# Kernel optimization log

Measured on AMD Instinct MI355X. Metric: run time of the kernel, lower is better.

## Reference

```python
import jax, jax.numpy as jnp
import numpy as np

D_MODEL = 1024
N_HEADS = 16
D_K = D_MODEL // N_HEADS


def setup_inputs() -> dict:
    key = jax.random.key(0)
    ks = jax.random.split(key, 9)
    B, S = 4, 2048
    scale = 0.02
    x = jax.random.normal(ks[0], (B, S, D_MODEL), dtype=jnp.float32)
    mask = jnp.ones((1, 1, S, S), dtype=jnp.int32)
    wq = jax.random.normal(ks[1], (D_MODEL, D_MODEL), dtype=jnp.float32) * scale
    bq = jnp.zeros((D_MODEL,), dtype=jnp.float32)
    wk = jax.random.normal(ks[2], (D_MODEL, D_MODEL), dtype=jnp.float32) * scale
    bk = jnp.zeros((D_MODEL,), dtype=jnp.float32)
    wv = jax.random.normal(ks[3], (D_MODEL, D_MODEL), dtype=jnp.float32) * scale
    bv = jnp.zeros((D_MODEL,), dtype=jnp.float32)
    wo = jax.random.normal(ks[4], (D_MODEL, D_MODEL), dtype=jnp.float32) * scale
    bo = jnp.zeros((D_MODEL,), dtype=jnp.float32)
    return {"x": x, "mask": mask, "wq": wq, "bq": bq, "wk": wk, "bk": bk,
            "wv": wv, "bv": bv, "wo": wo, "bo": bo}


def reference(x, mask, wq, bq, wk, bk, wv, bv, wo, bo):
    B, S, _ = x.shape
    # torch Linear: y = x @ W.T + b
    def proj(w, b):
        return (jnp.einsum('bsd,ed->bse', x, w) + b).reshape(B, S, N_HEADS, D_K).transpose(0, 2, 1, 3)
    q = proj(wq, bq)  # [B,H,S,Dk]
    k = proj(wk, bk)
    v = proj(wv, bv)
    scores = jnp.einsum('bhqd,bhkd->bhqk', q, k) / jnp.sqrt(jnp.float32(D_K))
    scores = jnp.where(mask == 0, jnp.float32(-jnp.inf), scores)
    attn = jax.nn.softmax(scores, axis=-1)
    out = jnp.einsum('bhqk,bhkd->bhqd', attn, v)  # [B,H,S,Dk]
    out = out.transpose(0, 2, 1, 3).reshape(B, S, D_MODEL)
    return jnp.einsum('bsd,ed->bse', out, wo) + bo
```

## Files before the change

kernel.cpp:

```cpp
#include <hip/hip_runtime.h>
#include <hip/hip_bf16.h>
#include <math.h>
#include <stdint.h>

typedef unsigned short u16;
typedef unsigned int u32;
typedef __bf16 bf16x2 __attribute__((ext_vector_type(2)));
typedef __bf16 bf16x8 __attribute__((ext_vector_type(8)));
typedef float f32x4 __attribute__((ext_vector_type(4)));

#define AS1 __attribute__((address_space(1)))
#define AS3 __attribute__((address_space(3)))

#define QSCALE 0.18033688011112042f

__device__ __forceinline__ u16 f2bf(float f) {
  union { float f; u32 i; } c; c.f = f;
  const u32 x = c.i;
  return (u16)((x + 0x7fffu + ((x >> 16) & 1u)) >> 16);
}
#if __has_builtin(__builtin_amdgcn_cvt_pk_bf16_f32)
__device__ __forceinline__ u32 pkbf(float a, float b) {
  const bf16x2 v = __builtin_amdgcn_cvt_pk_bf16_f32(a, b);
  union { bf16x2 v; u32 i; } c; c.v = v; return c.i;
}
#else
__device__ __forceinline__ u32 pkbf(float a, float b) {
  return (u32)f2bf(a) | ((u32)f2bf(b) << 16);
}
#endif
#if __has_builtin(__builtin_amdgcn_exp2f)
#define EXP2(x) __builtin_amdgcn_exp2f(x)
#else
#define EXP2(x) __expf((x) * 0.6931471805599453f)
#endif
__device__ __forceinline__ void gload_lds16(const void* g, void* lds) {
  __builtin_amdgcn_global_load_lds((const AS1 void*)g, (AS3 void*)lds, 16, 0, 0);
}

__global__ void cast_all_kernel(const float* __restrict__ x, const float* __restrict__ wq,
                                const float* __restrict__ wk, const float* __restrict__ wv,
                                const float* __restrict__ wo, u16* __restrict__ xh,
                                u16* __restrict__ wh) {
  const int i = blockIdx.x * 256 + threadIdx.x;
  const float* src; u16* dst; int off;
  if (i < 2097152) {
    src = x; dst = xh; off = i;
  } else {
    const int j = i - 2097152;
    const int w = j >> 18;
    off = j & 262143;
    src = (w == 0) ? wq : (w == 1) ? wk : (w == 2) ? wv : wo;
    dst = wh + (size_t)w * 1048576;
  }
  const float4 v = ((const float4*)src)[off];
  ushort4 o;
  o.x = f2bf(v.x); o.y = f2bf(v.y); o.z = f2bf(v.z); o.w = f2bf(v.w);
  ((ushort4*)dst)[off] = o;
}

template <int MODE, bool SCALE>
__device__ __forceinline__ void gemm_body(const u16* __restrict__ A,
                                          const u16* __restrict__ W,
                                          const float* __restrict__ bias,
                                          void* __restrict__ out) {
  __shared__ alignas(16) u16 As[128 * 32];
  __shared__ alignas(16) u16 Bs[128 * 32];
  const int tid = threadIdx.x;
  const int wave = tid >> 6, lane = tid & 63;
  const int quad = lane >> 4, l16 = lane & 15;
  const int lid = blockIdx.y * 8 + blockIdx.x;
  const int flat = ((lid & 7) << 6) | (lid >> 3);
  const int m0 = (flat >> 3) * 128, n0 = (flat & 7) * 128;
  const int wm = (wave >> 1) * 64, wn = (wave & 1) * 64;

  f32x4 vzero = {0.f, 0.f, 0.f, 0.f};
  f32x4 acc[4][4];
#pragma unroll
  for (int i = 0; i < 4; i++)
#pragma unroll
    for (int j = 0; j < 4; j++) acc[i][j] = vzero;

  for (int k0 = 0; k0 < 1024; k0 += 32) {
#pragma unroll
    for (int p = 0; p < 2; ++p) {
      const int cbase = p * 256 + wave * 64;
      const int c = cbase + lane;
      const int row = c >> 2, kc4 = c & 3;
      gload_lds16(A + (size_t)(m0 + row) * 1024 + k0 + kc4 * 8, (char*)As + cbase * 16);
      gload_lds16(W + (size_t)(n0 + row) * 1024 + k0 + kc4 * 8, (char*)Bs + cbase * 16);
    }
    __syncthreads();
    bf16x8 af[4], bw[4];
#pragma unroll
    for (int im = 0; im < 4; im++)
      af[im] = *(const bf16x8*)&As[(wm + im * 16 + l16) * 32 + quad * 8];
#pragma unroll
    for (int in_ = 0; in_ < 4; in_++)
      bw[in_] = *(const bf16x8*)&Bs[(wn + in_ * 16 + l16) * 32 + quad * 8];
#pragma unroll
    for (int im = 0; im < 4; im++)
#pragma unroll
      for (int in_ = 0; in_ < 4; in_++)
        acc[im][in_] = __builtin_amdgcn_mfma_f32_16x16x32_bf16(af[im], bw[in_], acc[im][in_], 0, 0, 0);
    __syncthreads();
  }

#pragma unroll
  for (int in_ = 0; in_ < 4; in_++) {
    const int col = n0 + wn + in_ * 16 + l16;
    const float bvf = bias[col];
    if (MODE == 2) {
      const int h = col >> 6, dk = col & 63;
#pragma unroll
      for (int im = 0; im < 4; im++) {
        const int row0 = m0 + wm + im * 16 + quad * 4;
        const int b = row0 >> 11, s = row0 & 2047;
        const u32 lo = pkbf(acc[im][in_][0] + bvf, acc[im][in_][1] + bvf);
        const u32 hi = pkbf(acc[im][in_][2] + bvf, acc[im][in_][3] + bvf);
        u16* base = (u16*)out + ((size_t)(b * 16 + h) * 64 + dk) * 2048 + s;
        uint2 pkd; pkd.x = lo; pkd.y = hi;
        *(uint2*)base = pkd;
      }
    } else {
#pragma unroll
      for (int im = 0; im < 4; im++) {
#pragma unroll
        for (int r = 0; r < 4; r++) {
          const int row = m0 + wm + im * 16 + quad * 4 + r;
          float v = acc[im][in_][r] + bvf;
          if (SCALE) v *= QSCALE;
          if (MODE == 0) {
            ((float*)out)[(size_t)row * 1024 + col] = v;
          } else {
            const int b = row >> 11, s = row & 2047;
            const int h = col >> 6, dk = col & 63;
            ((u16*)out)[((((size_t)b * 16 + h) * 2048) + s) * 64 + dk] = f2bf(v);
          }
        }
      }
    }
  }
}

__global__ __launch_bounds__(256) void gemm_qkv_kernel(
    const u16* __restrict__ x, const u16* __restrict__ wq, const u16* __restrict__ wk,
    const u16* __restrict__ wv, const float* __restrict__ bq, const float* __restrict__ bk,
    const float* __restrict__ bv, u16* __restrict__ Q, u16* __restrict__ K,
    u16* __restrict__ VT) {
  if (blockIdx.z == 0)      gemm_body<1, true >(x, wq, bq, Q);
  else if (blockIdx.z == 1) gemm_body<1, false>(x, wk, bk, K);
  else                      gemm_body<2, false>(x, wv, bv, VT);
}

__global__ __launch_bounds__(256) void gemm_o_kernel(const u16* __restrict__ A,
                                                     const u16* __restrict__ wo,
                                                     const float* __restrict__ bo,
                                                     float* __restrict__ out) {
  gemm_body<0, false>(A, wo, bo, out);
}

__global__ void mask_check_kernel(const int* __restrict__ mask, int* __restrict__ flag) {
  const int i = blockIdx.x * 256 + threadIdx.x;
  const int4 v = ((const int4*)mask)[i];
  if (v.x == 0 || v.y == 0 || v.z == 0 || v.w == 0) atomicOr(flag, 1);
}

__global__ __launch_bounds__(256) void attn_kernel(const u16* __restrict__ Q,
                                                   const u16* __restrict__ K,
                                                   const u16* __restrict__ VT,
                                                   const int* __restrict__ mask,
                                                   const int* __restrict__ flag,
                                                   u16* __restrict__ O) {
  __shared__ alignas(16) u16 Ks[64 * 64];
  __shared__ alignas(16) u16 Vt[64 * 64];
  __shared__ alignas(16) u16 Ps[4 * 2048];

  const int tid = threadIdx.x;
  const int wave = tid >> 6, lane = tid & 63;
  const int quad = lane >> 4, l16 = lane & 15;
  const int lid = blockIdx.y * 16 + blockIdx.x;
  const int flat = ((lid & 7) << 7) | (lid >> 3);
  const int qt_ = flat & 15, bh = flat >> 4;
  const int b = bh >> 4, h = bh & 15;
  const int q0 = qt_ * 128;
  const u16* Qh = Q + (size_t)bh * 2048 * 64;
  const u16* Kh = K + (size_t)bh * 2048 * 64;
  const u16* Vth = VT + (size_t)bh * 64 * 2048;
  u16* Pw = Ps + wave * 2048;
  const bool masked = (*flag != 0);

  bf16x8 aq[2][2];
#pragma unroll
  for (int qt = 0; qt < 2; qt++) {
    const u16* qrow = Qh + (size_t)(q0 + qt * 64 + wave * 16 + l16) * 64 + quad * 8;
    aq[qt][0] = *(const bf16x8*)qrow;
    aq[qt][1] = *(const bf16x8*)(qrow + 32);
  }

  f32x4 vzero = {0.f, 0.f, 0.f, 0.f};
  f32x4 acc[2][4];
#pragma unroll
  for (int qt = 0; qt < 2; qt++)
#pragma unroll
    for (int jd = 0; jd < 4; jd++) acc[qt][jd] = vzero;
  float lp[2][4] = {{0.f, 0.f, 0.f, 0.f}, {0.f, 0.f, 0.f, 0.f}};

  for (int kb = 0; kb < 32; ++kb) {
    const int key0 = kb * 64;
#pragma unroll
    for (int p = 0; p < 2; ++p) {
      const int cbase = p * 256 + wave * 64;
      const int c = cbase + lane;
      const int row = c >> 3, cc = c & 7;
      gload_lds16(Kh + (size_t)(key0 + row) * 64 + ((cc ^ (row & 7)) << 3),
                  (char*)Ks + cbase * 16);
      gload_lds16(Vth + (size_t)row * 2048 + key0 + ((cc ^ (row & 7)) << 3),
                  (char*)Vt + cbase * 16);
    }
    __syncthreads();

#pragma unroll
    for (int jn = 0; jn < 4; jn++) {
      f32x4 sc0 = vzero, sc1 = vzero;
      __builtin_amdgcn_s_setprio(1);
#pragma unroll
      for (int kc = 0; kc < 2; kc++) {
        const int r_ = jn * 16 + l16;
        const bf16x8 bk_ = *(const bf16x8*)
            &Ks[r_ * 64 + (((kc * 4 + quad) ^ (l16 & 7)) << 3)];
        sc0 = __builtin_amdgcn_mfma_f32_16x16x32_bf16(aq[0][kc], bk_, sc0, 0, 0, 0);
        sc1 = __builtin_amdgcn_mfma_f32_16x16x32_bf16(aq[1][kc], bk_, sc1, 0, 0, 0);
      }
      __builtin_amdgcn_s_setprio(0);
      if (masked) {
#pragma unroll
        for (int r = 0; r < 4; r++) {
          const int kg = key0 + jn * 16 + l16;
          const int qa = q0 + wave * 16 + quad * 4 + r;
          if (mask[(size_t)qa * 2048 + kg] == 0) sc0[r] = -INFINITY;
          if (mask[(size_t)(qa + 64) * 2048 + kg] == 0) sc1[r] = -INFINITY;
        }
      }
      float pe0[4], pe1[4];
#pragma unroll
      for (int r = 0; r < 4; r++) {
        pe0[r] = EXP2(sc0[r]); lp[0][r] += pe0[r];
        pe1[r] = EXP2(sc1[r]); lp[1][r] += pe1[r];
      }
#pragma unroll
      for (int r = 0; r < 4; r += 2) {
        const u32 pk0 = pkbf(pe0[r], pe0[r + 1]);
        const u32 pk1 = pkbf(pe1[r], pe1[r + 1]);
        const int qa = quad * 4 + r, qb = qa + 1;
        const int sw = jn * 2 + (l16 >> 3), lo3 = l16 & 7;
        Pw[qa * 64 + (((sw ^ (qa & 7)) << 3)) + lo3] = (u16)pk0;
        Pw[qb * 64 + (((sw ^ (qb & 7)) << 3)) + lo3] = (u16)(pk0 >> 16);
        Pw[(16 + qa) * 64 + (((sw ^ (qa & 7)) << 3)) + lo3] = (u16)pk1;
        Pw[(16 + qb) * 64 + (((sw ^ (qb & 7)) << 3)) + lo3] = (u16)(pk1 >> 16);
      }
    }

    bf16x8 ap0[2], ap1[2];
#pragma unroll
    for (int kc = 0; kc < 2; kc++) {
      ap0[kc] = *(const bf16x8*)&Pw[l16 * 64 + (((kc * 4 + quad) ^ (l16 & 7)) << 3)];
      ap1[kc] = *(const bf16x8*)&Pw[(16 + l16) * 64 + (((kc * 4 + quad) ^ (l16 & 7)) << 3)];
    }
    __builtin_amdgcn_s_setprio(1);
#pragma unroll
    for (int jd = 0; jd < 4; jd++) {
#pragma unroll
      for (int kc = 0; kc < 2; kc++) {
        const int dk_ = jd * 16 + l16;
        const bf16x8 bv_ = *(const bf16x8*)
            &Vt[dk_ * 64 + (((kc * 4 + quad) ^ (l16 & 7)) << 3)];
        acc[0][jd] = __builtin_amdgcn_mfma_f32_16x16x32_bf16(ap0[kc], bv_, acc[0][jd], 0, 0, 0);
        acc[1][jd] = __builtin_amdgcn_mfma_f32_16x16x32_bf16(ap1[kc], bv_, acc[1][jd], 0, 0, 0);
      }
    }
    __builtin_amdgcn_s_setprio(0);
    __syncthreads();
  }

#pragma unroll
  for (int qt = 0; qt < 2; qt++) {
#pragma unroll
    for (int r = 0; r < 4; r++) {
      float ls = lp[qt][r];
#pragma unroll
      for (int off = 1; off < 16; off <<= 1) ls += __shfl_xor(ls, off, 16);
      const float linv = 1.0f / ls;
      const int qg = q0 + qt * 64 + wave * 16 + quad * 4 + r;
      const size_t token = (size_t)b * 2048 + qg;
#pragma unroll
      for (int jd = 0; jd < 4; jd++) {
        const int col = h * 64 + jd * 16 + l16;
        O[token * 1024 + col] = f2bf(acc[qt][jd][r] * linv);
      }
    }
  }
}

extern "C" void kernel_launch(void* const* d_in, const int* in_sizes, int n_in,
                              void* d_out, int out_size, void* d_ws, size_t ws_size,
                              hipStream_t stream) {
  const float* x  = (const float*)d_in[0];
  const int* mask = (const int*)d_in[1];
  const float* wq = (const float*)d_in[2];
  const float* bq = (const float*)d_in[3];
  const float* wk = (const float*)d_in[4];
  const float* bk = (const float*)d_in[5];
  const float* wv = (const float*)d_in[6];
  const float* bv = (const float*)d_in[7];
  const float* wo = (const float*)d_in[8];
  const float* bo = (const float*)d_in[9];
  float* out = (float*)d_out;

  u16* xh = (u16*)d_ws;
  u16* wh = xh + 8388608;
  u16* Qw = wh + 4194304;
  u16* Kw = Qw + 8388608;
  u16* Vw = Kw + 8388608;
  int* mflag = (int*)(Vw + 8388608);
  u16* Ow = xh;

  hipMemsetAsync(mflag, 0, sizeof(int), stream);
  mask_check_kernel<<<4096, 256, 0, stream>>>(mask, mflag);
  cast_all_kernel<<<12288, 256, 0, stream>>>(x, wq, wk, wv, wo, xh, wh);

  gemm_qkv_kernel<<<dim3(8, 64, 3), 256, 0, stream>>>(
      xh, wh + 0 * 1048576, wh + 1 * 1048576, wh + 2 * 1048576,
      bq, bk, bv, Qw, Kw, Vw);
  attn_kernel<<<dim3(16, 64), 256, 0, stream>>>(Qw, Kw, Vw, mask, mflag, Ow);
  gemm_o_kernel<<<dim3(8, 64, 1), 256, 0, stream>>>(Ow, wh + 3 * 1048576, bo, out);
}
```

Measured before the change: 325.9 us.

## Deepen GEMM K-tile to 64 with XOR-swizzled LDS and fuse mask check into cast

The GEMM k-step grows from 32 to 64, which halves the number of barrier pairs per K loop. LDS rows are now XOR-swizzled in 16-byte chunks to avoid bank conflicts on the wider rows. The separate mask-check kernel is folded into the cast kernel as extra blocks, removing one launch. In exchange LDS use doubles per GEMM block, which may reduce occupancy.

```diff
diff --git a/kernel.cpp b/kernel.cpp
--- a/kernel.cpp
+++ b/kernel.cpp
@@ -40,9 +40,15 @@
 
 __global__ void cast_all_kernel(const float* __restrict__ x, const float* __restrict__ wq,
                                 const float* __restrict__ wk, const float* __restrict__ wv,
-                                const float* __restrict__ wo, u16* __restrict__ xh,
-                                u16* __restrict__ wh) {
+                                const float* __restrict__ wo, const int* __restrict__ mask,
+                                u16* __restrict__ xh, u16* __restrict__ wh,
+                                int* __restrict__ flag) {
   const int i = blockIdx.x * 256 + threadIdx.x;
+  if (i >= 3145728) {
+    const int4 v = ((const int4*)mask)[i - 3145728];
+    if (v.x == 0 || v.y == 0 || v.z == 0 || v.w == 0) atomicOr(flag, 1);
+    return;
+  }
   const float* src; u16* dst; int off;
   if (i < 2097152) {
     src = x; dst = xh; off = i;
@@ -64,8 +70,8 @@
                                           const u16* __restrict__ W,
                                           const float* __restrict__ bias,
                                           void* __restrict__ out) {
-  __shared__ alignas(16) u16 As[128 * 32];
-  __shared__ alignas(16) u16 Bs[128 * 32];
+  __shared__ alignas(16) u16 As[128 * 64];
+  __shared__ alignas(16) u16 Bs[128 * 64];
   const int tid = threadIdx.x;
   const int wave = tid >> 6, lane = tid & 63;
   const int quad = lane >> 4, l16 = lane & 15;
@@ -81,28 +87,36 @@
 #pragma unroll
     for (int j = 0; j < 4; j++) acc[i][j] = vzero;
 
-  for (int k0 = 0; k0 < 1024; k0 += 32) {
-#pragma unroll
-    for (int p = 0; p < 2; ++p) {
+  for (int k0 = 0; k0 < 1024; k0 += 64) {
+#pragma unroll
+    for (int p = 0; p < 4; ++p) {
       const int cbase = p * 256 + wave * 64;
       const int c = cbase + lane;
-      const int row = c >> 2, kc4 = c & 3;
-      gload_lds16(A + (size_t)(m0 + row) * 1024 + k0 + kc4 * 8, (char*)As + cbase * 16);
-      gload_lds16(W + (size_t)(n0 + row) * 1024 + k0 + kc4 * 8, (char*)Bs + cbase * 16);
+      const int row = c >> 3, cc = c & 7;
+      const int gcol = k0 + ((cc ^ (row & 7)) << 3);
+      gload_lds16(A + (size_t)(m0 + row) * 1024 + gcol, (char*)As + cbase * 16);
+      gload_lds16(W + (size_t)(n0 + row) * 1024 + gcol, (char*)Bs + cbase * 16);
     }
     __syncthreads();
-    bf16x8 af[4], bw[4];
-#pragma unroll
-    for (int im = 0; im < 4; im++)
-      af[im] = *(const bf16x8*)&As[(wm + im * 16 + l16) * 32 + quad * 8];
-#pragma unroll
-    for (int in_ = 0; in_ < 4; in_++)
-      bw[in_] = *(const bf16x8*)&Bs[(wn + in_ * 16 + l16) * 32 + quad * 8];
-#pragma unroll
-    for (int im = 0; im < 4; im++)
-#pragma unroll
-      for (int in_ = 0; in_ < 4; in_++)
-        acc[im][in_] = __builtin_amdgcn_mfma_f32_16x16x32_bf16(af[im], bw[in_], acc[im][in_], 0, 0, 0);
+#pragma unroll
+    for (int kk = 0; kk < 2; kk++) {
+      bf16x8 af[4], bw[4];
+#pragma unroll
+      for (int im = 0; im < 4; im++) {
+        const int r = wm + im * 16 + l16;
+        af[im] = *(const bf16x8*)&As[r * 64 + (((kk * 4 + quad) ^ (l16 & 7)) << 3)];
+      }
+#pragma unroll
+      for (int in_ = 0; in_ < 4; in_++) {
+        const int r = wn + in_ * 16 + l16;
+        bw[in_] = *(const bf16x8*)&Bs[r * 64 + (((kk * 4 + quad) ^ (l16 & 7)) << 3)];
+      }
+#pragma unroll
+      for (int im = 0; im < 4; im++)
+#pragma unroll
+        for (int in_ = 0; in_ < 4; in_++)
+          acc[im][in_] = __builtin_amdgcn_mfma_f32_16x16x32_bf16(af[im], bw[in_], acc[im][in_], 0, 0, 0);
+    }
     __syncthreads();
   }
 
@@ -158,12 +172,6 @@
                                                      const float* __restrict__ bo,
                                                      float* __restrict__ out) {
   gemm_body<0, false>(A, wo, bo, out);
-}
-
-__global__ void mask_check_kernel(const int* __restrict__ mask, int* __restrict__ flag) {
-  const int i = blockIdx.x * 256 + threadIdx.x;
-  const int4 v = ((const int4*)mask)[i];
-  if (v.x == 0 || v.y == 0 || v.z == 0 || v.w == 0) atomicOr(flag, 1);
 }
 
 __global__ __launch_bounds__(256) void attn_kernel(const u16* __restrict__ Q,
@@ -326,8 +334,7 @@
   u16* Ow = xh;
 
   hipMemsetAsync(mflag, 0, sizeof(int), stream);
-  mask_check_kernel<<<4096, 256, 0, stream>>>(mask, mflag);
-  cast_all_kernel<<<12288, 256, 0, stream>>>(x, wq, wk, wv, wo, xh, wh);
+  cast_all_kernel<<<16384, 256, 0, stream>>>(x, wq, wk, wv, wo, mask, xh, wh, mflag);
 
   gemm_qkv_kernel<<<dim3(8, 64, 3), 256, 0, stream>>>(
       xh, wh + 0 * 1048576, wh + 1 * 1048576, wh + 2 * 1048576,
```

Result: slower. 366.0 us (+12.3%).
